# Optimization experiments

Measured on AMD Instinct MI355X. Metric: run time of the kernel, lower is better.

Reference implementation:

```python
import jax, jax.numpy as jnp
import numpy as np

H = 1024      # hidden_size
NH = 16       # num_attention_heads
HD = H // NH  # head_size
DF = 4096     # ff intermediate
EPS = 1e-5


def layer_norm(x, g, b):
    mu = jnp.mean(x, axis=-1, keepdims=True)
    var = jnp.var(x, axis=-1, keepdims=True)
    return (x - mu) * jax.lax.rsqrt(var + EPS) * g + b


def setup_inputs() -> dict:
    key = jax.random.key(0)
    ks = jax.random.split(key, 4)
    s = 0.02
    return {
        "x": jax.random.normal(ks[0], (2, 2048, H), dtype=jnp.float32),
        "w_qkv": jax.random.normal(ks[1], (H, 3 * H), dtype=jnp.float32) * s,
        "ln1_g": jnp.ones((H,), jnp.float32),
        "ln1_b": jnp.zeros((H,), jnp.float32),
        "w1": jax.random.normal(ks[2], (H, DF), dtype=jnp.float32) * s,
        "b1": jnp.zeros((DF,), jnp.float32),
        "w2": jax.random.normal(ks[3], (DF, H), dtype=jnp.float32) * s,
        "b2": jnp.zeros((H,), jnp.float32),
        "ln2_g": jnp.ones((H,), jnp.float32),
        "ln2_b": jnp.zeros((H,), jnp.float32),
    }


def reference(x, w_qkv, ln1_g, ln1_b, w1, b1, w2, b2, ln2_g, ln2_b):
    b, s, h = x.shape
    # --- MHSelfAttention (naive) ---
    qkv = x @ w_qkv                                   # [b, s, 3h]
    qkv = qkv.reshape(b, s, 3, NH, HD)
    q, k, v = (jnp.moveaxis(qkv, 2, 0)                # [3, b, s, nh, hd]
               .transpose(0, 1, 3, 2, 4))             # [3, b, nh, s, hd]
    # NOTE: faithful quirk — scaled by sqrt(hidden_size), not head_size
    scores = jnp.einsum('bnqd,bnkd->bnqk', q, k) / jnp.sqrt(jnp.float32(h))
    probs = jax.nn.softmax(scores, axis=-1)
    ctx = jnp.einsum('bnqk,bnkd->bnqd', probs, v)     # [b, nh, s, hd]
    attn_out = ctx.transpose(0, 2, 1, 3).reshape(b, s, h)
    # post-norm residual (dropout = identity in eval)
    x = x + layer_norm(attn_out, ln1_g, ln1_b)
    # --- FFN ---
    ff = jax.nn.relu(x @ w1 + b1) @ w2 + b2
    x = x + layer_norm(ff, ln2_g, ln2_b)
    return x
```

## Files before the change

### kernel.cpp

```cpp
#include <hip/hip_runtime.h>


typedef unsigned short u16;
typedef unsigned int u32;
typedef __bf16 bf16x8 __attribute__((ext_vector_type(8)));
typedef float f32x4 __attribute__((ext_vector_type(4)));
typedef u32 u32x4 __attribute__((ext_vector_type(4)));
typedef u16 u16x4 __attribute__((ext_vector_type(4)));

__device__ __forceinline__ u16 f2b(float f) {
  u32 u = __builtin_bit_cast(u32, f);
  u += 0x7fffu + ((u >> 16) & 1u);
  return (u16)(u >> 16);
}
__device__ __forceinline__ float b2f(u16 u) {
  return __builtin_bit_cast(float, (u32)u << 16);
}

__device__ __forceinline__ void gld_lds16(const u16* g, u16* l) {
  __builtin_amdgcn_global_load_lds(
      (const __attribute__((address_space(1))) u32*)g,
      (__attribute__((address_space(3))) u32*)l, 16, 0, 0);
}

__global__ __launch_bounds__(256) void convert_bf16_kernel(
    const float* __restrict__ in, u16* __restrict__ out) {
  const int idx = blockIdx.x * 256 + threadIdx.x;
  float4 v = ((const float4*)in)[idx];
  u16x4 o = { f2b(v.x), f2b(v.y), f2b(v.z), f2b(v.w) };
  ((u16x4*)out)[idx] = o;
}

__global__ __launch_bounds__(256) void transpose_bf16_kernel(
    const float* __restrict__ in, u16* __restrict__ out, int R, int C) {
  __shared__ float tile[32][33];
  const int cb = blockIdx.x * 32, rb = blockIdx.y * 32;
  const int c = threadIdx.x & 31;
  const int r0 = threadIdx.x >> 5;
#pragma unroll
  for (int rr = 0; rr < 32; rr += 8)
    tile[r0 + rr][c] = in[(size_t)(rb + r0 + rr) * C + cb + c];
  __syncthreads();
#pragma unroll
  for (int rr = 0; rr < 32; rr += 8)
    out[(size_t)(cb + r0 + rr) * R + rb + c] = f2b(tile[c][r0 + rr]);
}

__global__ __launch_bounds__(256) void transpose_v_kernel(
    const u16* __restrict__ qkv, u16* __restrict__ vt) {
  __shared__ u16 t[64][70];
  const int bh = blockIdx.x, st = blockIdx.y;
  const int b = bh >> 4, nh = bh & 15;
  const int s0 = st * 64;
  const int r = threadIdx.x >> 3, c = (threadIdx.x & 7) << 3;
  const u16* src = qkv + (size_t)(b * 2048 + s0) * 3072 + 2048 + nh * 64;
#pragma unroll
  for (int rr = 0; rr < 64; rr += 32)
    *(u32x4*)&t[r + rr][c] = *(const u32x4*)(src + (size_t)(r + rr) * 3072 + c);
  __syncthreads();
  u16* dst = vt + ((size_t)bh * 64) * 2048 + s0;
#pragma unroll
  for (int rr = 0; rr < 64; rr += 32) {
    const int d = r + rr;
    u16 tmp[8];
#pragma unroll
    for (int j = 0; j < 8; ++j) tmp[j] = t[c + j][d];
    *(u32x4*)(dst + (size_t)d * 2048 + c) = *(u32x4*)tmp;
  }
}

__global__ __launch_bounds__(256) void gemm_bt_kernel(
    const u16* __restrict__ A, const u16* __restrict__ Bt,
    const float* __restrict__ bias, float* __restrict__ Cf, u16* __restrict__ Cb,
    int M, int N, int K, int relu,
    u16* __restrict__ Cb1, u16* __restrict__ Cb2, u16* __restrict__ Cb3) {
  const int bid = blockIdx.x;
  const int xcd = bid & 7;
  const int g = bid >> 3;
  const int m0 = (xcd * 4 + (g & 3)) * 128;
  const int n0 = (g >> 2) * 128;
  const int z = blockIdx.y;
  const int kn = K / (int)gridDim.y;
  if (z == 1) Cb = Cb1; else if (z == 2) Cb = Cb2; else if (z == 3) Cb = Cb3;
  const int tid = threadIdx.x;
  const int w = tid >> 6, lane = tid & 63, quad = lane >> 4, l16 = lane & 15;
  const int wm = (w & 1) * 64, wn = (w >> 1) * 64;

  __shared__ u16 As[2][128][32];
  __shared__ u16 Bs[2][128][32];

  f32x4 acc[4][4];
#pragma unroll
  for (int i = 0; i < 4; ++i)
#pragma unroll
    for (int j = 0; j < 4; ++j) acc[i][j] = {0.f, 0.f, 0.f, 0.f};

  const int srow = w * 16 + (lane >> 2);
  const int scol = (lane & 3) << 3;
  const u16* Ag = A + (size_t)(m0 + srow) * K + scol + (size_t)z * kn;
  const u16* Bg = Bt + (size_t)(n0 + srow) * K + scol + (size_t)z * kn;
  const size_t rstep = (size_t)64 * K;

  for (int k0 = 0; k0 < kn; k0 += 64) {
    __syncthreads();
    gld_lds16(Ag + k0,              &As[0][w * 16][0]);
    gld_lds16(Ag + k0 + 32,         &As[1][w * 16][0]);
    gld_lds16(Ag + rstep + k0,      &As[0][64 + w * 16][0]);
    gld_lds16(Ag + rstep + k0 + 32, &As[1][64 + w * 16][0]);
    gld_lds16(Bg + k0,              &Bs[0][w * 16][0]);
    gld_lds16(Bg + k0 + 32,         &Bs[1][w * 16][0]);
    gld_lds16(Bg + rstep + k0,      &Bs[0][64 + w * 16][0]);
    gld_lds16(Bg + rstep + k0 + 32, &Bs[1][64 + w * 16][0]);
    __syncthreads();

#pragma unroll
    for (int s = 0; s < 2; ++s) {
      bf16x8 af[4], bfr[4];
#pragma unroll
      for (int i = 0; i < 4; ++i)
        af[i] = *(const bf16x8*)&As[s][wm + i * 16 + l16][quad * 8];
#pragma unroll
      for (int j = 0; j < 4; ++j)
        bfr[j] = *(const bf16x8*)&Bs[s][wn + j * 16 + l16][quad * 8];
#pragma unroll
      for (int i = 0; i < 4; ++i)
#pragma unroll
        for (int j = 0; j < 4; ++j)
          acc[i][j] = __builtin_amdgcn_mfma_f32_16x16x32_bf16(af[i], bfr[j], acc[i][j], 0, 0, 0);
    }
  }

#pragma unroll
  for (int i = 0; i < 4; ++i) {
    const int row = m0 + wm + i * 16 + quad * 4;
#pragma unroll
    for (int j = 0; j < 4; ++j) {
      const int col = n0 + wn + j * 16 + l16;
      const float bv = bias ? bias[col] : 0.f;
#pragma unroll
      for (int r = 0; r < 4; ++r) {
        float v = acc[i][j][r] + bv;
        if (relu) v = fmaxf(v, 0.f);
        const size_t idx = (size_t)(row + r) * N + col;
        if (Cf) Cf[idx] = v;
        if (Cb) Cb[idx] = f2b(v);
      }
    }
  }
}

__global__ __launch_bounds__(256, 4) void attn_kernel(
    const u16* __restrict__ qkv, const u16* __restrict__ vt,
    float* __restrict__ Op0, float* __restrict__ Op1,
    float* __restrict__ lpart) {
  const int bh = blockIdx.x;
  const int qt = blockIdx.y;
  const int kz = blockIdx.z;
  const int b = bh >> 4, nh = bh & 15;
  const int tid = threadIdx.x;
  const int w = tid >> 6, lane = tid & 63, quad = lane >> 4, l16 = lane & 15;
  const float c2 = 0.04508422f;

  __shared__ u16 KH[2][64][32];
  __shared__ u16 VH[2][64][32];
  __shared__ u16 QP[4][32][68];

  u16 (*Qs)[68] = (u16(*)[68])&QP[0][0][0];

  const size_t rs = 3072;
  const u16* qbase = qkv + (size_t)b * 2048 * rs + nh * 64;
  const u16* kbase = qbase + 1024;
  const u16* vbase = vt + (size_t)bh * 64 * 2048;
  const int q0 = qt * 128;
  const int k0beg = kz * 1024;

  {
    const int row = tid >> 1, colb = (tid & 1) << 5;
#pragma unroll
    for (int h = 0; h < 4; ++h) {
      u32x4 v = *(const u32x4*)(qbase + (size_t)(q0 + row) * rs + colb + h * 8);
      u16 ti[8], to[8];
      *(u32x4*)ti = v;
#pragma unroll
      for (int j = 0; j < 8; ++j) to[j] = f2b(b2f(ti[j]) * c2);
      *(u32x4*)&Qs[row][colb + h * 8] = *(u32x4*)to;
    }
  }
  __syncthreads();

  bf16x8 aq[2][2];
#pragma unroll
  for (int mi = 0; mi < 2; ++mi)
#pragma unroll
    for (int d0 = 0; d0 < 2; ++d0)
      aq[mi][d0] = *(const bf16x8*)&Qs[w * 32 + mi * 16 + l16][d0 * 32 + quad * 8];

  bf16x8 ones;
#pragma unroll
  for (int j = 0; j < 8; ++j) ones[j] = (__bf16)1.0f;

  f32x4 Oacc[2][4], l_acc[2];
#pragma unroll
  for (int mi = 0; mi < 2; ++mi) {
    l_acc[mi] = {0.f, 0.f, 0.f, 0.f};
#pragma unroll
    for (int jt = 0; jt < 4; ++jt) Oacc[mi][jt] = {0.f, 0.f, 0.f, 0.f};
  }

  const int drow = lane >> 2;
  const int dcol = (lane & 3) << 3;

#pragma unroll 1
  for (int t = 0; t < 16; ++t) {
    const int k0 = k0beg + t * 64;
    __syncthreads();
    gld_lds16(kbase + (size_t)(k0 + w * 16 + drow) * rs + dcol,        &KH[0][w * 16][0]);
    gld_lds16(kbase + (size_t)(k0 + w * 16 + drow) * rs + 32 + dcol,   &KH[1][w * 16][0]);
    gld_lds16(vbase + (size_t)(w * 16 + drow) * 2048 + k0 + dcol,      &VH[0][w * 16][0]);
    gld_lds16(vbase + (size_t)(w * 16 + drow) * 2048 + k0 + 32 + dcol, &VH[1][w * 16][0]);
    __syncthreads();

    f32x4 S[2][4];
#pragma unroll
    for (int mi = 0; mi < 2; ++mi)
#pragma unroll
      for (int jt = 0; jt < 4; ++jt) S[mi][jt] = {0.f, 0.f, 0.f, 0.f};
#pragma unroll
    for (int d0 = 0; d0 < 2; ++d0)
#pragma unroll
      for (int jt = 0; jt < 4; ++jt) {
        bf16x8 bv = *(const bf16x8*)&KH[d0][jt * 16 + l16][quad * 8];
        S[0][jt] = __builtin_amdgcn_mfma_f32_16x16x32_bf16(aq[0][d0], bv, S[0][jt], 0, 0, 0);
        S[1][jt] = __builtin_amdgcn_mfma_f32_16x16x32_bf16(aq[1][d0], bv, S[1][jt], 0, 0, 0);
      }

#pragma unroll
    for (int mi = 0; mi < 2; ++mi)
#pragma unroll
      for (int jt = 0; jt < 4; ++jt)
#pragma unroll
        for (int r = 0; r < 4; ++r) {
          float p = exp2f(S[mi][jt][r]);
          QP[w][mi * 16 + quad * 4 + r][jt * 16 + l16] =
              (u16)(__builtin_bit_cast(u32, p) >> 16);
        }

    bf16x8 ap[2][2];
#pragma unroll
    for (int mi = 0; mi < 2; ++mi)
#pragma unroll
      for (int kk = 0; kk < 2; ++kk)
        ap[mi][kk] = *(const bf16x8*)&QP[w][mi * 16 + l16][kk * 32 + quad * 8];
#pragma unroll
    for (int kk = 0; kk < 2; ++kk) {
#pragma unroll
      for (int jt = 0; jt < 4; ++jt) {
        bf16x8 bv = *(const bf16x8*)&VH[kk][jt * 16 + l16][quad * 8];
        Oacc[0][jt] = __builtin_amdgcn_mfma_f32_16x16x32_bf16(ap[0][kk], bv, Oacc[0][jt], 0, 0, 0);
        Oacc[1][jt] = __builtin_amdgcn_mfma_f32_16x16x32_bf16(ap[1][kk], bv, Oacc[1][jt], 0, 0, 0);
      }
      l_acc[0] = __builtin_amdgcn_mfma_f32_16x16x32_bf16(ap[0][kk], ones, l_acc[0], 0, 0, 0);
      l_acc[1] = __builtin_amdgcn_mfma_f32_16x16x32_bf16(ap[1][kk], ones, l_acc[1], 0, 0, 0);
    }
  }

  float* opart = kz ? Op1 : Op0;
  float* obase = opart + (size_t)b * 2048 * 1024 + (size_t)nh * 64;
  float* lbase = lpart + (size_t)kz * 4096 * 16 + (size_t)b * 2048 * 16 + nh;
#pragma unroll
  for (int mi = 0; mi < 2; ++mi) {
    const int qrow = q0 + w * 32 + mi * 16 + quad * 4;
#pragma unroll
    for (int r = 0; r < 4; ++r) {
#pragma unroll
      for (int jt = 0; jt < 4; ++jt)
        obase[(size_t)(qrow + r) * 1024 + jt * 16 + l16] = Oacc[mi][jt][r];
      if (l16 == 0) lbase[(size_t)(qrow + r) * 16] = l_acc[mi][r];
    }
  }
}

__global__ __launch_bounds__(256) void ln_attn_kernel(
    const float* __restrict__ O0, const float* __restrict__ O1,
    const float* __restrict__ l0, const float* __restrict__ l1,
    const float* __restrict__ xres, const float* __restrict__ g,
    const float* __restrict__ bb, float* __restrict__ outf,
    u16* __restrict__ outb) {
  const int row = blockIdx.x;
  const int tid = threadIdx.x;
  const int w = tid >> 6, lane = tid & 63;
  const int head = tid >> 4;
  float4 a0 = ((const float4*)(O0 + (size_t)row * 1024))[tid];
  float4 a1 = ((const float4*)(O1 + (size_t)row * 1024))[tid];
  const float inv = 1.f / (l0[row * 16 + head] + l1[row * 16 + head]);
  float4 v;
  v.x = (a0.x + a1.x) * inv;
  v.y = (a0.y + a1.y) * inv;
  v.z = (a0.z + a1.z) * inv;
  v.w = (a0.w + a1.w) * inv;
  float s = v.x + v.y + v.z + v.w;
  float s2 = v.x * v.x + v.y * v.y + v.z * v.z + v.w * v.w;
#pragma unroll
  for (int off = 32; off > 0; off >>= 1) {
    s += __shfl_xor(s, off);
    s2 += __shfl_xor(s2, off);
  }
  __shared__ float red[8];
  if (lane == 0) { red[w] = s; red[4 + w] = s2; }
  __syncthreads();
  s = red[0] + red[1] + red[2] + red[3];
  s2 = red[4] + red[5] + red[6] + red[7];
  const float mu = s * (1.f / 1024.f);
  const float var = s2 * (1.f / 1024.f) - mu * mu;
  const float rstd = rsqrtf(var + 1e-5f);
  float4 xr = ((const float4*)(xres + (size_t)row * 1024))[tid];
  float4 gv = ((const float4*)g)[tid];
  float4 bv = ((const float4*)bb)[tid];
  float4 o;
  o.x = xr.x + (v.x - mu) * rstd * gv.x + bv.x;
  o.y = xr.y + (v.y - mu) * rstd * gv.y + bv.y;
  o.z = xr.z + (v.z - mu) * rstd * gv.z + bv.z;
  o.w = xr.w + (v.w - mu) * rstd * gv.w + bv.w;
  ((float4*)(outf + (size_t)row * 1024))[tid] = o;
  u16x4 ob = { f2b(o.x), f2b(o.y), f2b(o.z), f2b(o.w) };
  *(u16x4*)(outb + (size_t)row * 1024 + (size_t)tid * 4) = ob;
}

__global__ __launch_bounds__(256) void ln_ffn_kernel(
    const u16* __restrict__ p0, const u16* __restrict__ p1,
    const u16* __restrict__ p2, const u16* __restrict__ p3,
    const float* __restrict__ bias, const float* __restrict__ xres,
    const float* __restrict__ g, const float* __restrict__ bb,
    float* __restrict__ outf) {
  const int row = blockIdx.x;
  const int tid = threadIdx.x;
  const int w = tid >> 6, lane = tid & 63;
  u16x4 a0 = ((const u16x4*)(p0 + (size_t)row * 1024))[tid];
  u16x4 a1 = ((const u16x4*)(p1 + (size_t)row * 1024))[tid];
  u16x4 a2 = ((const u16x4*)(p2 + (size_t)row * 1024))[tid];
  u16x4 a3 = ((const u16x4*)(p3 + (size_t)row * 1024))[tid];
  float4 bv4 = ((const float4*)bias)[tid];
  float4 v;
  v.x = (b2f(a0[0]) + b2f(a1[0])) + (b2f(a2[0]) + b2f(a3[0])) + bv4.x;
  v.y = (b2f(a0[1]) + b2f(a1[1])) + (b2f(a2[1]) + b2f(a3[1])) + bv4.y;
  v.z = (b2f(a0[2]) + b2f(a1[2])) + (b2f(a2[2]) + b2f(a3[2])) + bv4.z;
  v.w = (b2f(a0[3]) + b2f(a1[3])) + (b2f(a2[3]) + b2f(a3[3])) + bv4.w;
  float s = v.x + v.y + v.z + v.w;
  float s2 = v.x * v.x + v.y * v.y + v.z * v.z + v.w * v.w;
#pragma unroll
  for (int off = 32; off > 0; off >>= 1) {
    s += __shfl_xor(s, off);
    s2 += __shfl_xor(s2, off);
  }
  __shared__ float red[8];
  if (lane == 0) { red[w] = s; red[4 + w] = s2; }
  __syncthreads();
  s = red[0] + red[1] + red[2] + red[3];
  s2 = red[4] + red[5] + red[6] + red[7];
  const float mu = s * (1.f / 1024.f);
  const float var = s2 * (1.f / 1024.f) - mu * mu;
  const float rstd = rsqrtf(var + 1e-5f);
  float4 xr = ((const float4*)(xres + (size_t)row * 1024))[tid];
  float4 gv = ((const float4*)g)[tid];
  float4 bv = ((const float4*)bb)[tid];
  float4 o;
  o.x = xr.x + (v.x - mu) * rstd * gv.x + bv.x;
  o.y = xr.y + (v.y - mu) * rstd * gv.y + bv.y;
  o.z = xr.z + (v.z - mu) * rstd * gv.z + bv.z;
  o.w = xr.w + (v.w - mu) * rstd * gv.w + bv.w;
  ((float4*)(outf + (size_t)row * 1024))[tid] = o;
}

extern "C" void kernel_launch(void* const* d_in, const int* in_sizes, int n_in,
                              void* d_out, int out_size, void* d_ws, size_t ws_size,
                              hipStream_t stream) {
  const float* x     = (const float*)d_in[0];
  const float* w_qkv = (const float*)d_in[1];
  const float* ln1_g = (const float*)d_in[2];
  const float* ln1_b = (const float*)d_in[3];
  const float* w1    = (const float*)d_in[4];
  const float* b1    = (const float*)d_in[5];
  const float* w2    = (const float*)d_in[6];
  const float* b2    = (const float*)d_in[7];
  const float* ln2_g = (const float*)d_in[8];
  const float* ln2_b = (const float*)d_in[9];
  float* out = (float*)d_out;
  char* ws = (char*)d_ws;

  u16*   xb    = (u16*)(ws + 0);
  u16*   wqkvT = (u16*)(ws + 8388608);
  u16*   qkvb  = (u16*)(ws + 31457280);
  u16*   vT    = (u16*)(ws + 56623104);
  float* Op0   = (float*)(ws + 0);
  float* Op1   = (float*)(ws + 73400320);
  float* lp    = (float*)(ws + 90177536);
  float* x1    = (float*)(ws + 31457280);
  u16*   x1b   = (u16*)(ws + 48234496);
  u16*   w1T   = (u16*)(ws + 14680064);
  u16*   w2T   = (u16*)(ws + 23068672);
  u16*   h1    = (u16*)(ws + 56623104);
  u16*   fp0   = (u16*)(ws + 0);
  u16*   fp1   = (u16*)(ws + 8388608);
  u16*   fp2   = (u16*)(ws + 48234496);
  u16*   fp3   = (u16*)(ws + 90177536);

  convert_bf16_kernel<<<4096, 256, 0, stream>>>(x, xb);
  transpose_bf16_kernel<<<dim3(96, 32), 256, 0, stream>>>(w_qkv, wqkvT, 1024, 3072);

  gemm_bt_kernel<<<dim3(32 * 24, 1), 256, 0, stream>>>(
      xb, wqkvT, nullptr, nullptr, qkvb, 4096, 3072, 1024, 0,
      nullptr, nullptr, nullptr);
  transpose_v_kernel<<<dim3(32, 32), 256, 0, stream>>>(qkvb, vT);
  attn_kernel<<<dim3(32, 16, 2), 256, 0, stream>>>(qkvb, vT, Op0, Op1, lp);

  ln_attn_kernel<<<4096, 256, 0, stream>>>(
      Op0, Op1, lp, lp + 4096 * 16, x, ln1_g, ln1_b, x1, x1b);

  transpose_bf16_kernel<<<dim3(128, 32), 256, 0, stream>>>(w1, w1T, 1024, 4096);
  transpose_bf16_kernel<<<dim3(32, 128), 256, 0, stream>>>(w2, w2T, 4096, 1024);

  gemm_bt_kernel<<<dim3(32 * 32, 1), 256, 0, stream>>>(
      x1b, w1T, b1, nullptr, h1, 4096, 4096, 1024, 1,
      nullptr, nullptr, nullptr);
  gemm_bt_kernel<<<dim3(32 * 8, 4), 256, 0, stream>>>(
      h1, w2T, nullptr, nullptr, fp0, 4096, 1024, 4096, 0,
      fp1, fp2, fp3);

  ln_ffn_kernel<<<4096, 256, 0, stream>>>(
      fp0, fp1, fp2, fp3, b2, x1, ln2_g, ln2_b, out);
}
```

Baseline: 354.3 us.

## Restructure attention to 32x32x16 MFMA with register-resident P via permlane swap

Rewrites the attention inner loop to use 32x32x16 bf16 MFMAs, computing S transposed (K as A operand, Q as B) so the exponentiated probabilities can be packed with v_cvt_pk_bf16_f32 and rearranged by v_permlane32_swap into the A-operand layout for the PV MFMA. This removes the per-tile round trip of P through LDS and the separate Q staging in shared memory. The row-sum is now accumulated with scalar adds plus one cross-half shuffle instead of extra MFMAs against a ones vector. K/V tiles move to XOR-swizzled 64x64 LDS arrays to avoid bank conflicts, and the cost is a more intricate lane mapping that must match the MFMA register layout exactly.

```diff
diff --git a/kernel.cpp b/kernel.cpp
--- a/kernel.cpp
+++ b/kernel.cpp
@@ -5,6 +5,7 @@
 typedef unsigned int u32;
 typedef __bf16 bf16x8 __attribute__((ext_vector_type(8)));
 typedef float f32x4 __attribute__((ext_vector_type(4)));
+typedef float f32x16 __attribute__((ext_vector_type(16)));
 typedef u32 u32x4 __attribute__((ext_vector_type(4)));
 typedef u16 u16x4 __attribute__((ext_vector_type(4)));
 
@@ -15,6 +16,12 @@
 }
 __device__ __forceinline__ float b2f(u16 u) {
   return __builtin_bit_cast(float, (u32)u << 16);
+}
+
+__device__ __forceinline__ u32 cvtpk(float lo, float hi) {
+  u32 r;
+  asm("v_cvt_pk_bf16_f32 %0, %1, %2" : "=v"(r) : "v"(lo), "v"(hi));
+  return r;
 }
 
 __device__ __forceinline__ void gld_lds16(const u16* g, u16* l) {
@@ -158,14 +165,12 @@
   const int kz = blockIdx.z;
   const int b = bh >> 4, nh = bh & 15;
   const int tid = threadIdx.x;
-  const int w = tid >> 6, lane = tid & 63, quad = lane >> 4, l16 = lane & 15;
+  const int w = tid >> 6, lane = tid & 63;
+  const int l32 = lane & 31, hi = lane >> 5;
   const float c2 = 0.04508422f;
 
-  __shared__ u16 KH[2][64][32];
-  __shared__ u16 VH[2][64][32];
-  __shared__ u16 QP[4][32][68];
-
-  u16 (*Qs)[68] = (u16(*)[68])&QP[0][0][0];
+  __shared__ u16 KS[64][64];
+  __shared__ u16 VS[64][64];
 
   const size_t rs = 3072;
   const u16* qbase = qkv + (size_t)b * 2048 * rs + nh * 64;
@@ -174,110 +179,103 @@
   const int q0 = qt * 128;
   const int k0beg = kz * 1024;
 
+  bf16x8 aq[4];
   {
-    const int row = tid >> 1, colb = (tid & 1) << 5;
-#pragma unroll
-    for (int h = 0; h < 4; ++h) {
-      u32x4 v = *(const u32x4*)(qbase + (size_t)(q0 + row) * rs + colb + h * 8);
+    const u16* qrow = qbase + (size_t)(q0 + w * 32 + l32) * rs + hi * 8;
+#pragma unroll
+    for (int ds = 0; ds < 4; ++ds) {
+      u32x4 v = *(const u32x4*)(qrow + ds * 16);
       u16 ti[8], to[8];
       *(u32x4*)ti = v;
 #pragma unroll
       for (int j = 0; j < 8; ++j) to[j] = f2b(b2f(ti[j]) * c2);
-      *(u32x4*)&Qs[row][colb + h * 8] = *(u32x4*)to;
-    }
-  }
-  __syncthreads();
-
-  bf16x8 aq[2][2];
-#pragma unroll
-  for (int mi = 0; mi < 2; ++mi)
-#pragma unroll
-    for (int d0 = 0; d0 < 2; ++d0)
-      aq[mi][d0] = *(const bf16x8*)&Qs[w * 32 + mi * 16 + l16][d0 * 32 + quad * 8];
-
-  bf16x8 ones;
-#pragma unroll
-  for (int j = 0; j < 8; ++j) ones[j] = (__bf16)1.0f;
-
-  f32x4 Oacc[2][4], l_acc[2];
-#pragma unroll
-  for (int mi = 0; mi < 2; ++mi) {
-    l_acc[mi] = {0.f, 0.f, 0.f, 0.f};
-#pragma unroll
-    for (int jt = 0; jt < 4; ++jt) Oacc[mi][jt] = {0.f, 0.f, 0.f, 0.f};
-  }
-
-  const int drow = lane >> 2;
-  const int dcol = (lane & 3) << 3;
+      u32x4 pk = *(u32x4*)to;
+      aq[ds] = __builtin_bit_cast(bf16x8, pk);
+    }
+  }
+
+  f32x16 Oacc[2];
+#pragma unroll
+  for (int dn = 0; dn < 2; ++dn)
+#pragma unroll
+    for (int i = 0; i < 16; ++i) Oacc[dn][i] = 0.f;
+  float ls[4] = {0.f, 0.f, 0.f, 0.f};
+
+  const int srow = lane >> 3;
+  const int scol = ((lane & 7) ^ srow) << 3;
 
 #pragma unroll 1
   for (int t = 0; t < 16; ++t) {
     const int k0 = k0beg + t * 64;
     __syncthreads();
-    gld_lds16(kbase + (size_t)(k0 + w * 16 + drow) * rs + dcol,        &KH[0][w * 16][0]);
-    gld_lds16(kbase + (size_t)(k0 + w * 16 + drow) * rs + 32 + dcol,   &KH[1][w * 16][0]);
-    gld_lds16(vbase + (size_t)(w * 16 + drow) * 2048 + k0 + dcol,      &VH[0][w * 16][0]);
-    gld_lds16(vbase + (size_t)(w * 16 + drow) * 2048 + k0 + 32 + dcol, &VH[1][w * 16][0]);
+    gld_lds16(kbase + (size_t)(k0 + w * 16 + srow) * rs + scol,       &KS[w * 16][0]);
+    gld_lds16(kbase + (size_t)(k0 + w * 16 + 8 + srow) * rs + scol,   &KS[w * 16 + 8][0]);
+    gld_lds16(vbase + (size_t)(w * 16 + srow) * 2048 + k0 + scol,     &VS[w * 16][0]);
+    gld_lds16(vbase + (size_t)(w * 16 + 8 + srow) * 2048 + k0 + scol, &VS[w * 16 + 8][0]);
     __syncthreads();
 
-    f32x4 S[2][4];
-#pragma unroll
-    for (int mi = 0; mi < 2; ++mi)
-#pragma unroll
-      for (int jt = 0; jt < 4; ++jt) S[mi][jt] = {0.f, 0.f, 0.f, 0.f};
-#pragma unroll
-    for (int d0 = 0; d0 < 2; ++d0)
-#pragma unroll
-      for (int jt = 0; jt < 4; ++jt) {
-        bf16x8 bv = *(const bf16x8*)&KH[d0][jt * 16 + l16][quad * 8];
-        S[0][jt] = __builtin_amdgcn_mfma_f32_16x16x32_bf16(aq[0][d0], bv, S[0][jt], 0, 0, 0);
-        S[1][jt] = __builtin_amdgcn_mfma_f32_16x16x32_bf16(aq[1][d0], bv, S[1][jt], 0, 0, 0);
+    f32x16 S[2];
+#pragma unroll
+    for (int jt = 0; jt < 2; ++jt)
+#pragma unroll
+      for (int i = 0; i < 16; ++i) S[jt][i] = 0.f;
+#pragma unroll
+    for (int jt = 0; jt < 2; ++jt) {
+      const int krow = jt * 32 + l32;
+#pragma unroll
+      for (int ds = 0; ds < 4; ++ds) {
+        bf16x8 kv = *(const bf16x8*)&KS[krow][((2 * ds + hi) ^ (krow & 7)) << 3];
+        S[jt] = __builtin_amdgcn_mfma_f32_32x32x16_bf16(kv, aq[ds], S[jt], 0, 0, 0);
       }
-
-#pragma unroll
-    for (int mi = 0; mi < 2; ++mi)
-#pragma unroll
-      for (int jt = 0; jt < 4; ++jt)
-#pragma unroll
-        for (int r = 0; r < 4; ++r) {
-          float p = exp2f(S[mi][jt][r]);
-          QP[w][mi * 16 + quad * 4 + r][jt * 16 + l16] =
-              (u16)(__builtin_bit_cast(u32, p) >> 16);
-        }
-
-    bf16x8 ap[2][2];
-#pragma unroll
-    for (int mi = 0; mi < 2; ++mi)
-#pragma unroll
-      for (int kk = 0; kk < 2; ++kk)
-        ap[mi][kk] = *(const bf16x8*)&QP[w][mi * 16 + l16][kk * 32 + quad * 8];
-#pragma unroll
-    for (int kk = 0; kk < 2; ++kk) {
-#pragma unroll
-      for (int jt = 0; jt < 4; ++jt) {
-        bf16x8 bv = *(const bf16x8*)&VH[kk][jt * 16 + l16][quad * 8];
-        Oacc[0][jt] = __builtin_amdgcn_mfma_f32_16x16x32_bf16(ap[0][kk], bv, Oacc[0][jt], 0, 0, 0);
-        Oacc[1][jt] = __builtin_amdgcn_mfma_f32_16x16x32_bf16(ap[1][kk], bv, Oacc[1][jt], 0, 0, 0);
+    }
+
+    bf16x8 pa[4];
+#pragma unroll
+    for (int jt = 0; jt < 2; ++jt) {
+      float p[16];
+#pragma unroll
+      for (int r = 0; r < 16; ++r) {
+        p[r] = exp2f(S[jt][r]);
+        ls[r & 3] += p[r];
       }
-      l_acc[0] = __builtin_amdgcn_mfma_f32_16x16x32_bf16(ap[0][kk], ones, l_acc[0], 0, 0, 0);
-      l_acc[1] = __builtin_amdgcn_mfma_f32_16x16x32_bf16(ap[1][kk], ones, l_acc[1], 0, 0, 0);
-    }
-  }
+#pragma unroll
+      for (int bq = 0; bq < 2; ++bq) {
+        u32 x0 = cvtpk(p[8 * bq + 0], p[8 * bq + 1]);
+        u32 y0 = cvtpk(p[8 * bq + 4], p[8 * bq + 5]);
+        u32 x1 = cvtpk(p[8 * bq + 2], p[8 * bq + 3]);
+        u32 y1 = cvtpk(p[8 * bq + 6], p[8 * bq + 7]);
+        asm("v_permlane32_swap_b32 %0, %1" : "+v"(x0), "+v"(y0));
+        asm("v_permlane32_swap_b32 %0, %1" : "+v"(x1), "+v"(y1));
+        u32x4 dw = {x0, x1, y0, y1};
+        pa[2 * jt + bq] = __builtin_bit_cast(bf16x8, dw);
+      }
+    }
+
+#pragma unroll
+    for (int dn = 0; dn < 2; ++dn) {
+      const int vrow = dn * 32 + l32;
+#pragma unroll
+      for (int ks = 0; ks < 4; ++ks) {
+        bf16x8 vv = *(const bf16x8*)&VS[vrow][((2 * ks + hi) ^ (vrow & 7)) << 3];
+        Oacc[dn] = __builtin_amdgcn_mfma_f32_32x32x16_bf16(pa[ks], vv, Oacc[dn], 0, 0, 0);
+      }
+    }
+  }
+
+  float lsum = (ls[0] + ls[1]) + (ls[2] + ls[3]);
+  const float ltot = lsum + __shfl_xor(lsum, 32);
 
   float* opart = kz ? Op1 : Op0;
   float* obase = opart + (size_t)b * 2048 * 1024 + (size_t)nh * 64;
   float* lbase = lpart + (size_t)kz * 4096 * 16 + (size_t)b * 2048 * 16 + nh;
 #pragma unroll
-  for (int mi = 0; mi < 2; ++mi) {
-    const int qrow = q0 + w * 32 + mi * 16 + quad * 4;
-#pragma unroll
-    for (int r = 0; r < 4; ++r) {
-#pragma unroll
-      for (int jt = 0; jt < 4; ++jt)
-        obase[(size_t)(qrow + r) * 1024 + jt * 16 + l16] = Oacc[mi][jt][r];
-      if (l16 == 0) lbase[(size_t)(qrow + r) * 16] = l_acc[mi][r];
-    }
-  }
+  for (int r = 0; r < 16; ++r) {
+    const int qrow = q0 + w * 32 + (r & 3) + 8 * (r >> 2) + 4 * hi;
+#pragma unroll
+    for (int dn = 0; dn < 2; ++dn)
+      obase[(size_t)qrow * 1024 + dn * 32 + l32] = Oacc[dn][r];
+  }
+  if (lane < 32) lbase[(size_t)(q0 + w * 32 + l32) * 16] = ltot;
 }
 
 __global__ __launch_bounds__(256) void ln_attn_kernel(
```

Result: faster. 344.8 us (-2.7%).
